# Kernel tuning notes

Hardware: AMD Instinct MI355X
Metric: run time of the kernel (lower is better)

The kernel has to match this reference:

```python
import jax, jax.numpy as jnp
import numpy as np

DIM, HEADS, HEAD_DIM = 1024, 16, 64
B, S = 2, 1024
LAMBDA = 4.0
EPS = 1e-6


def setup_inputs() -> dict:
    key = jax.random.key(0)
    ks = jax.random.split(key, 7)
    sc = 1.0 / np.sqrt(DIM)
    return {
        "x": jax.random.normal(ks[0], (B, S, DIM), jnp.float32),
        "qkv_w": jax.random.normal(ks[1], (3 * DIM, DIM), jnp.float32) * sc,
        "qkv_b": jax.random.normal(ks[2], (3 * DIM,), jnp.float32) * 0.01,
        "proj_w": jax.random.normal(ks[3], (DIM, DIM), jnp.float32) * sc,
        "proj_b": jax.random.normal(ks[4], (DIM,), jnp.float32) * 0.01,
        "dwc_w": jax.random.normal(ks[5], (DIM, 1, 3), jnp.float32) * 0.3,
        "dwc_b": jax.random.normal(ks[6], (DIM,), jnp.float32) * 0.01,
    }


def _l1_dist(q, k):
    # q,k: [B,H,S,Dh] -> pairwise L1 distance [B,H,S,S].
    # Accumulate over head_dim with a (rematerialized) scan so we never
    # materialize the [B,H,S,S,Dh] broadcast tensor.
    qT = jnp.moveaxis(q, -1, 0)  # [Dh,B,H,S]
    kT = jnp.moveaxis(k, -1, 0)

    def step(acc, qk):
        qd, kd = qk  # [B,H,S]
        return acc + jnp.abs(qd[..., :, None] - kd[..., None, :]), None

    init = jnp.zeros(q.shape[:-1] + (k.shape[-2],), q.dtype)
    dist, _ = jax.lax.scan(jax.checkpoint(step), init, (qT, kT))
    return dist


def reference(x, qkv_w, qkv_b, proj_w, proj_b, dwc_w, dwc_b):
    Bq, Sq, C = x.shape
    # qkv projection -> q,k,v each [B,H,S,Dh]
    qkv = (x @ qkv_w.T + qkv_b).reshape(Bq, Sq, 3, HEADS, HEAD_DIM)
    qkv = jnp.transpose(qkv, (2, 0, 3, 1, 4))
    q, k, v = qkv[0], qkv[1], qkv[2]

    # exact Laplacian (L1-distance) kernel attention, row-normalized
    dist = _l1_dist(q, k)                       # [B,H,S,S]
    kern = jnp.exp(-LAMBDA * dist / HEAD_DIM)   # mean-L1 scaling
    attn = kern / (jnp.sum(kern, axis=-1, keepdims=True) + EPS)
    global_attn = jnp.einsum("bhij,bhjd->bhid", attn, v)

    # depthwise conv1d local branch on v (channel order = head-major)
    v1d = jnp.transpose(v, (0, 1, 3, 2)).reshape(Bq, C, Sq)  # [B,C,S]
    local = jax.lax.conv_general_dilated(
        v1d, dwc_w, window_strides=(1,), padding=((1, 1),),
        feature_group_count=C, dimension_numbers=("NCH", "OIH", "NCH"))
    local = local + dwc_b[None, :, None]
    local = jnp.transpose(local.reshape(Bq, HEADS, HEAD_DIM, Sq), (0, 1, 3, 2))

    y = global_attn + local                      # [B,H,S,Dh]
    y = jnp.transpose(y, (0, 2, 1, 3)).reshape(Bq, Sq, C)
    return y @ proj_w.T + proj_b
```

## Files before the change

### kernel.cpp

```cpp
#include <hip/hip_runtime.h>

#define DIMC 1024
#define HEADS 16
#define HD 64
#define BATCH 2
#define SEQ 1024
#define NQKV 3072

typedef _Float16 f16;
typedef _Float16 half8 __attribute__((ext_vector_type(8)));
typedef _Float16 half4v __attribute__((ext_vector_type(4)));
typedef float floatx4 __attribute__((ext_vector_type(4)));

__device__ __forceinline__ void gld16(const void* g, void* l) {
  __builtin_amdgcn_global_load_lds((const __attribute__((address_space(1))) void*)g,
                                   (__attribute__((address_space(3))) void*)l, 16, 0, 0);
}

__device__ __forceinline__ unsigned sadU8(unsigned a, unsigned b, unsigned c) {
#if __has_builtin(__builtin_amdgcn_sad_u8)
  return __builtin_amdgcn_sad_u8(a, b, c);
#else
  unsigned d;
  asm("v_sad_u8 %0, %1, %2, %3" : "=v"(d) : "v"(a), "v"(b), "v"(c));
  return d;
#endif
}

__global__ __launch_bounds__(256) void cvt_kernel(
    const float* __restrict__ x, const float* __restrict__ wq, const float* __restrict__ wp,
    f16* __restrict__ x16, f16* __restrict__ wq16, f16* __restrict__ wp16)
{
  int bid = blockIdx.x;
  const float* src; f16* dst; int base;
  if (bid < 512)        { src = x;  dst = x16;  base = bid; }
  else if (bid < 1280)  { src = wq; dst = wq16; base = bid - 512; }
  else                  { src = wp; dst = wp16; base = bid - 1280; }
  long long i0 = (long long)base*1024 + threadIdx.x;
#pragma unroll
  for (int k2 = 0; k2 < 4; ++k2) {
    long long i = i0 + k2*256;
    float4 v = ((const float4*)src)[i];
    half4v h; h[0]=(f16)v.x; h[1]=(f16)v.y; h[2]=(f16)v.z; h[3]=(f16)v.w;
    *(half4v*)(dst + i*4) = h;
  }
}

template<int TM, int TN, int BK, int MW, int MODE>
__global__ __launch_bounds__(256, MW) void gemm_kernel(
    const f16* __restrict__ A, const f16* __restrict__ Bw, const float* __restrict__ bias,
    unsigned char* __restrict__ q8, unsigned char* __restrict__ k8, f16* __restrict__ vT,
    float* __restrict__ outp, int K)
{
  constexpr int MT = TM / 32;
  constexpr int NT = TN / 32;
  constexpr int G  = BK / 8;
  __shared__ f16 As[TM*BK];
  __shared__ f16 Bs[TN*BK];
  const int tid = threadIdx.x;
  const int wave = tid >> 6, lane = tid & 63;
  const int lq = lane >> 4, li = lane & 15;
  const int m0 = blockIdx.y * TM, n0 = blockIdx.x * TN;
  const int wm = (wave & 1) * (TM/2), wn = (wave >> 1) * (TN/2);
  floatx4 acc[MT][NT] = {};

  const int kIters = K / BK;
  for (int kt = 0; kt < kIters; ++kt) {
    __syncthreads();
#pragma unroll
    for (int r = 0; r < TM*BK/2048; ++r) {
      int slot = r*256 + tid;
      int row = slot / G, c = slot % G, g = c ^ (row & (G-1));
      gld16(A + (size_t)(m0+row)*K + kt*BK + g*8, As + slot*8);
    }
#pragma unroll
    for (int r = 0; r < TN*BK/2048; ++r) {
      int slot = r*256 + tid;
      int row = slot / G, c = slot % G, g = c ^ (row & (G-1));
      gld16(Bw + (size_t)(n0+row)*K + kt*BK + g*8, Bs + slot*8);
    }
    __syncthreads();
#pragma unroll
    for (int ks = 0; ks < BK/32; ++ks) {
      half8 af[MT], bf[NT];
      int kc = ks*4 + lq;
#pragma unroll
      for (int t = 0; t < MT; ++t) {
        int am = wm + t*16 + li;
        af[t] = *(const half8*)&As[am*BK + (kc ^ (am & (G-1)))*8];
      }
#pragma unroll
      for (int t = 0; t < NT; ++t) {
        int bn = wn + t*16 + li;
        bf[t] = *(const half8*)&Bs[bn*BK + (kc ^ (bn & (G-1)))*8];
      }
#pragma unroll
      for (int mt = 0; mt < MT; ++mt)
#pragma unroll
        for (int nt = 0; nt < NT; ++nt)
          acc[mt][nt] = __builtin_amdgcn_mfma_f32_16x16x32_f16(af[mt], bf[nt], acc[mt][nt], 0, 0, 0);
    }
  }

#pragma unroll
  for (int mt = 0; mt < MT; ++mt) {
#pragma unroll
    for (int nt = 0; nt < NT; ++nt) {
      int f = n0 + wn + nt*16 + li;
      float bb = bias[f];
      if (MODE == 0) {
        int which = f >> 10, cc = f & 1023, h = cc >> 6, d = cc & 63;
        int t0 = m0 + wm + mt*16 + lq*4;
        int b = t0 >> 10, s0 = t0 & 1023;
        if (which == 2) {
          half4v hv;
#pragma unroll
          for (int r = 0; r < 4; ++r) hv[r] = (f16)(acc[mt][nt][r] + bb);
          *(half4v*)&vT[((size_t)((b*HEADS + h)*HD + d))*SEQ + s0] = hv;
        } else {
          unsigned char* dst = (which == 0) ? q8 : k8;
#pragma unroll
          for (int r = 0; r < 4; ++r) {
            float v = acc[mt][nt][r] + bb;
            int u = (int)floorf(v * 16.0f + 128.5f);
            u = u < 0 ? 0 : (u > 255 ? 255 : u);
            dst[((size_t)((b*HEADS + h)*SEQ + s0 + r))*HD + d] = (unsigned char)u;
          }
        }
      } else {
#pragma unroll
        for (int r = 0; r < 4; ++r) {
          int t = m0 + wm + mt*16 + lq*4 + r;
          outp[(size_t)t*DIMC + f] = acc[mt][nt][r] + bb;
        }
      }
    }
  }
}

__global__ __launch_bounds__(256, 3) void attn_kernel(
    const unsigned char* __restrict__ q8g, const unsigned char* __restrict__ k8g,
    const f16* __restrict__ vTg, const float* __restrict__ dwcw, const float* __restrict__ dwcb,
    f16* __restrict__ y16)
{
  __shared__ unsigned char q8s[32*64];
  __shared__ unsigned char k8s[2][128*64];
  __shared__ f16 sfrag[2][8*64*8];
  __shared__ float rspart[32*16];
  __shared__ float rowsum[32];

  const int tid = threadIdx.x;
  const int lin = blockIdx.x + 16 * blockIdx.y;
  const int bh = (lin & 7) * 4 + ((lin >> 3) & 3);
  const int i0 = (lin >> 5) * 32;
  const int lane = tid & 63, wave = tid >> 6;
  const int lq = lane >> 4, li = lane & 15;
  const int iL = tid & 15, jt = tid >> 4;
  const int ksj = jt >> 2, qj = jt & 3;
  const int scs = jt & 3;

  {
    if (tid < 128)
      gld16(q8g + ((size_t)(bh*SEQ) + i0)*HD + tid*16, q8s + tid*16);
#pragma unroll
    for (int r = 0; r < 2; ++r) {
      int slot = r*256 + tid;
      int row = slot >> 2, c4 = slot & 3, sc4 = c4 ^ ((row >> 3) & 3);
      gld16(k8g + ((size_t)(bh*SEQ) + row)*HD + sc4*16, k8s[0] + slot*16);
    }
  }
  __syncthreads();

  unsigned qr[2][16];
#pragma unroll
  for (int n = 0; n < 2; ++n)
#pragma unroll
    for (int c4 = 0; c4 < 4; ++c4) {
      uint4 t = *(const uint4*)&q8s[(iL + n*16)*64 + c4*16];
      qr[n][c4*4+0] = t.x; qr[n][c4*4+1] = t.y; qr[n][c4*4+2] = t.z; qr[n][c4*4+3] = t.w;
    }

  float rs[2] = {0.f, 0.f};
  floatx4 pacc[2] = {};
  const f16* vbase = vTg + ((size_t)(bh*HD) + wave*16 + li)*SEQ;

  for (int jb = 0; jb < 8; ++jb) {
    const int j0 = jb * 128;
    const int cur = jb & 1;

    if (jb < 7) {
#pragma unroll
      for (int r = 0; r < 2; ++r) {
        int slot = r*256 + tid;
        int row = slot >> 2, c4 = slot & 3, sc4 = c4 ^ ((row >> 3) & 3);
        gld16(k8g + ((size_t)(bh*SEQ) + j0 + 128 + row)*HD + sc4*16,
              k8s[cur ^ 1] + slot*16);
      }
    }
    half8 vfrag[4];
#pragma unroll
    for (int ks = 0; ks < 4; ++ks)
      vfrag[ks] = *(const half8*)(vbase + j0 + (ks*4 + lq)*8);

    unsigned sacc[2][8] = {};
#pragma unroll
    for (int c4 = 0; c4 < 4; ++c4) {
      uint4 kk[8];
#pragma unroll
      for (int jj = 0; jj < 8; ++jj)
        kk[jj] = *(const uint4*)&k8s[cur][(jt*8 + jj)*64 + ((c4 ^ scs) << 4)];
#pragma unroll
      for (int n = 0; n < 2; ++n)
#pragma unroll
        for (int jj = 0; jj < 8; ++jj) {
          sacc[n][jj] = sadU8(qr[n][c4*4+0], kk[jj].x, sacc[n][jj]);
          sacc[n][jj] = sadU8(qr[n][c4*4+1], kk[jj].y, sacc[n][jj]);
          sacc[n][jj] = sadU8(qr[n][c4*4+2], kk[jj].z, sacc[n][jj]);
          sacc[n][jj] = sadU8(qr[n][c4*4+3], kk[jj].w, sacc[n][jj]);
        }
    }
#pragma unroll
    for (int n = 0; n < 2; ++n) {
      half8 sv;
#pragma unroll
      for (int jj = 0; jj < 8; ++jj) {
        float sf = exp2f(-0.0056355275f * (float)sacc[n][jj]);
        rs[n] += sf;
        sv[jj] = (f16)sf;
      }
      *(half8*)&sfrag[cur][((n*4 + ksj)*64 + qj*16 + iL)*8] = sv;
    }
    __syncthreads();

#pragma unroll
    for (int ks = 0; ks < 4; ++ks) {
      half8 a0 = *(const half8*)&sfrag[cur][((0*4 + ks)*64 + lane)*8];
      half8 a1 = *(const half8*)&sfrag[cur][((1*4 + ks)*64 + lane)*8];
      pacc[0] = __builtin_amdgcn_mfma_f32_16x16x32_f16(a0, vfrag[ks], pacc[0], 0, 0, 0);
      pacc[1] = __builtin_amdgcn_mfma_f32_16x16x32_f16(a1, vfrag[ks], pacc[1], 0, 0, 0);
    }
  }

#pragma unroll
  for (int n = 0; n < 2; ++n) rspart[(iL + n*16)*16 + jt] = rs[n];
  __syncthreads();
  if (tid < 32) {
    float s = 0.f;
#pragma unroll
    for (int t = 0; t < 16; ++t) s += rspart[tid*16 + t];
    rowsum[tid] = s + 1e-6f;
  }
  __syncthreads();

  const int b = bh >> 4, h = bh & 15;
  {
    int d = wave*16 + li;
    int c = h*64 + d;
    float w0 = dwcw[c*3+0], w1 = dwcw[c*3+1], w2 = dwcw[c*3+2], cb = dwcb[c];
    const f16* vrow = vTg + ((size_t)(bh*HD) + d)*SEQ;
#pragma unroll
    for (int mt = 0; mt < 2; ++mt) {
      int s0 = i0 + mt*16 + lq*4;
      float vv[6];
#pragma unroll
      for (int e = 0; e < 6; ++e) {
        int s = s0 - 1 + e;
        vv[e] = (s >= 0 && s < SEQ) ? (float)vrow[s] : 0.f;
      }
#pragma unroll
      for (int r = 0; r < 4; ++r) {
        int ii = mt*16 + lq*4 + r;
        float val = pacc[mt][r] / rowsum[ii];
        val += w0*vv[r] + w1*vv[r+1] + w2*vv[r+2] + cb;
        int s = i0 + ii;
        y16[((size_t)(b*SEQ + s))*DIMC + c] = (f16)val;
      }
    }
  }
}

extern "C" void kernel_launch(void* const* d_in, const int* in_sizes, int n_in,
                              void* d_out, int out_size, void* d_ws, size_t ws_size,
                              hipStream_t stream) {
  const float* x      = (const float*)d_in[0];
  const float* qkv_w  = (const float*)d_in[1];
  const float* qkv_b  = (const float*)d_in[2];
  const float* proj_w = (const float*)d_in[3];
  const float* proj_b = (const float*)d_in[4];
  const float* dwc_w  = (const float*)d_in[5];
  const float* dwc_b  = (const float*)d_in[6];
  float* out = (float*)d_out;

  char* ws = (char*)d_ws;
  f16* x16  = (f16*)(ws);
  f16* wq16 = (f16*)(ws + (4ll<<20));
  f16* wp16 = (f16*)(ws + (10ll<<20));
  unsigned char* q8 = (unsigned char*)(ws + (12ll<<20));
  unsigned char* k8 = (unsigned char*)(ws + (14ll<<20));
  f16* vT   = (f16*)(ws + (16ll<<20));
  f16* y16  = (f16*)(ws + (20ll<<20));

  cvt_kernel<<<1536, 256, 0, stream>>>(x, qkv_w, proj_w, x16, wq16, wp16);
  gemm_kernel<128,128,128,2,0><<<dim3(24, 16), 256, 0, stream>>>(x16, wq16, qkv_b, q8, k8, vT, nullptr, DIMC);
  attn_kernel<<<dim3(16, 64), 256, 0, stream>>>(q8, k8, vT, dwc_w, dwc_b, y16);
  gemm_kernel<64,64,256,2,1><<<dim3(16, 32), 256, 0, stream>>>(y16, wp16, proj_b, nullptr, nullptr, nullptr, out, DIMC);
}
```

Before: 147.1 us.

## Double-buffer LDS tiles in GEMM kernel to overlap loads with MFMA

Splits the GEMM shared-memory tiles into two buffers and prefetches the next K-slice with global_load_lds while MFMAs consume the current one, leaving a single barrier per iteration. The K-tile depth is halved for both GEMM launches so total LDS use stays the same. This aims to hide global-to-LDS latency behind compute. In exchange there are more iterations, each with a barrier, and the two GEMMs are likely a small share of total time next to the attention kernel.

```diff
diff --git a/kernel.cpp b/kernel.cpp
--- a/kernel.cpp
+++ b/kernel.cpp
@@ -55,8 +55,8 @@
   constexpr int MT = TM / 32;
   constexpr int NT = TN / 32;
   constexpr int G  = BK / 8;
-  __shared__ f16 As[TM*BK];
-  __shared__ f16 Bs[TN*BK];
+  __shared__ f16 As[2][TM*BK];
+  __shared__ f16 Bs[2][TN*BK];
   const int tid = threadIdx.x;
   const int wave = tid >> 6, lane = tid & 63;
   const int lq = lane >> 4, li = lane & 15;
@@ -65,21 +65,29 @@
   floatx4 acc[MT][NT] = {};
 
   const int kIters = K / BK;
+
+#define GEMM_STAGE(buf, kt)                                                     \
+  {                                                                             \
+    _Pragma("unroll")                                                           \
+    for (int r = 0; r < TM*BK/2048; ++r) {                                      \
+      int slot = r*256 + tid;                                                   \
+      int row = slot / G, c = slot % G, g = c ^ (row & (G-1));                  \
+      gld16(A + (size_t)(m0+row)*K + (kt)*BK + g*8, As[buf] + slot*8);          \
+    }                                                                           \
+    _Pragma("unroll")                                                           \
+    for (int r = 0; r < TN*BK/2048; ++r) {                                      \
+      int slot = r*256 + tid;                                                   \
+      int row = slot / G, c = slot % G, g = c ^ (row & (G-1));                  \
+      gld16(Bw + (size_t)(n0+row)*K + (kt)*BK + g*8, Bs[buf] + slot*8);         \
+    }                                                                           \
+  }
+
+  GEMM_STAGE(0, 0);
+  __syncthreads();
+
   for (int kt = 0; kt < kIters; ++kt) {
-    __syncthreads();
-#pragma unroll
-    for (int r = 0; r < TM*BK/2048; ++r) {
-      int slot = r*256 + tid;
-      int row = slot / G, c = slot % G, g = c ^ (row & (G-1));
-      gld16(A + (size_t)(m0+row)*K + kt*BK + g*8, As + slot*8);
-    }
-#pragma unroll
-    for (int r = 0; r < TN*BK/2048; ++r) {
-      int slot = r*256 + tid;
-      int row = slot / G, c = slot % G, g = c ^ (row & (G-1));
-      gld16(Bw + (size_t)(n0+row)*K + kt*BK + g*8, Bs + slot*8);
-    }
-    __syncthreads();
+    const int cur = kt & 1;
+    if (kt + 1 < kIters) GEMM_STAGE(cur ^ 1, kt + 1);
 #pragma unroll
     for (int ks = 0; ks < BK/32; ++ks) {
       half8 af[MT], bf[NT];
@@ -87,12 +95,12 @@
 #pragma unroll
       for (int t = 0; t < MT; ++t) {
         int am = wm + t*16 + li;
-        af[t] = *(const half8*)&As[am*BK + (kc ^ (am & (G-1)))*8];
+        af[t] = *(const half8*)&As[cur][am*BK + (kc ^ (am & (G-1)))*8];
       }
 #pragma unroll
       for (int t = 0; t < NT; ++t) {
         int bn = wn + t*16 + li;
-        bf[t] = *(const half8*)&Bs[bn*BK + (kc ^ (bn & (G-1)))*8];
+        bf[t] = *(const half8*)&Bs[cur][bn*BK + (kc ^ (bn & (G-1)))*8];
       }
 #pragma unroll
       for (int mt = 0; mt < MT; ++mt)
@@ -100,7 +108,9 @@
         for (int nt = 0; nt < NT; ++nt)
           acc[mt][nt] = __builtin_amdgcn_mfma_f32_16x16x32_f16(af[mt], bf[nt], acc[mt][nt], 0, 0, 0);
     }
-  }
+    __syncthreads();
+  }
+#undef GEMM_STAGE
 
 #pragma unroll
   for (int mt = 0; mt < MT; ++mt) {
@@ -301,7 +311,7 @@
   f16* y16  = (f16*)(ws + (20ll<<20));
 
   cvt_kernel<<<1536, 256, 0, stream>>>(x, qkv_w, proj_w, x16, wq16, wp16);
-  gemm_kernel<128,128,128,2,0><<<dim3(24, 16), 256, 0, stream>>>(x16, wq16, qkv_b, q8, k8, vT, nullptr, DIMC);
+  gemm_kernel<128,128,64,2,0><<<dim3(24, 16), 256, 0, stream>>>(x16, wq16, qkv_b, q8, k8, vT, nullptr, DIMC);
   attn_kernel<<<dim3(16, 64), 256, 0, stream>>>(q8, k8, vT, dwc_w, dwc_b, y16);
-  gemm_kernel<64,64,256,2,1><<<dim3(16, 32), 256, 0, stream>>>(y16, wp16, proj_b, nullptr, nullptr, nullptr, out, DIMC);
-}
+  gemm_kernel<64,64,128,2,1><<<dim3(16, 32), 256, 0, stream>>>(y16, wp16, proj_b, nullptr, nullptr, nullptr, out, DIMC);
+}
```

After: 150.0 us. About the same (+2.0%).
